# Performance work log

Hardware: AMD Instinct MI355X
Metric: run time of the kernel (lower is better)

Reference implementation:

```python
import jax, jax.numpy as jnp
import numpy as np

N, E, D_IN, HEADS, C = 100000, 1600000, 128, 4, 32  # C = out_channels per head


def setup_inputs() -> dict:
    key = jax.random.key(0)
    ks = jax.random.split(key, 10)
    s = 1.0 / np.sqrt(D_IN)
    return {
        "x": jax.random.normal(ks[0], (N, D_IN), jnp.float32),
        "edge_index": jax.random.randint(ks[1], (2, E), 0, N, jnp.int64),
        "Wq": jax.random.normal(ks[2], (D_IN, HEADS * C), jnp.float32) * s,
        "bq": jnp.zeros((HEADS * C,), jnp.float32),
        "Wk": jax.random.normal(ks[3], (D_IN, HEADS * C), jnp.float32) * s,
        "bk": jnp.zeros((HEADS * C,), jnp.float32),
        "Wv": jax.random.normal(ks[4], (D_IN, HEADS * C), jnp.float32) * s,
        "bv": jnp.zeros((HEADS * C,), jnp.float32),
        "Wskip": jax.random.normal(ks[5], (D_IN, HEADS * C), jnp.float32) * s,
        "bskip": jnp.zeros((HEADS * C,), jnp.float32),
    }


def reference(x, edge_index, Wq, bq, Wk, bk, Wv, bv, Wskip, bskip):
    n = x.shape[0]
    src, dst = edge_index[0], edge_index[1]  # message flows src (j) -> dst (i)
    q = (x @ Wq + bq).reshape(n, HEADS, C)
    k = (x @ Wk + bk).reshape(n, HEADS, C)
    v = (x @ Wv + bv).reshape(n, HEADS, C)

    # per-edge attention logits [E, H]
    alpha = jnp.einsum('ehc,ehc->eh', q[dst], k[src]) / jnp.sqrt(jnp.float32(C))

    # segment softmax over incoming edges of each target node
    m = jax.ops.segment_max(alpha, dst, num_segments=n)          # [N, H]
    p = jnp.exp(alpha - m[dst])                                   # [E, H]
    z = jax.ops.segment_sum(p, dst, num_segments=n)               # [N, H]
    w = p / (z[dst] + 1e-16)                                      # [E, H]

    # softmax-weighted scatter aggregation of values
    out = jax.ops.segment_sum(v[src] * w[:, :, None], dst, num_segments=n)
    out = out.reshape(n, HEADS * C)

    # root/skip connection (beta=False default: plain add)
    out = out + x @ Wskip + bskip
    return out
```

## Files before the change

kernel.cpp:

```cpp
#include <hip/hip_runtime.h>

#define DIN 128
#define NHEADS 4
#define CH 32
#define MT 64
#define NPB 256
#define EPB_IT 25
#define FB_CAP 6144

#define ST_H 136

typedef _Float16 h8 __attribute__((ext_vector_type(8)));
typedef _Float16 h2 __attribute__((ext_vector_type(2)));
typedef float f4 __attribute__((ext_vector_type(4)));

__global__ __launch_bounds__(256) void prep_w(
    const float* __restrict__ Wq, const float* __restrict__ Wk,
    const float* __restrict__ Wv, const float* __restrict__ Wsk,
    _Float16* __restrict__ wt)
{
    int i = blockIdx.x * 256 + threadIdx.x;
    if (i >= 4 * 16384) return;
    int mat = i >> 14;
    int rem = i & 16383;
    int n  = rem >> 7;
    int kk = rem & 127;
    const float* W = (mat == 0) ? Wq : (mat == 1) ? Wk : (mat == 2) ? Wv : Wsk;
    wt[i] = (_Float16)W[kk * 128 + n];
}

__global__ __launch_bounds__(256) void qkvs_mat(
    const float* __restrict__ x, const _Float16* __restrict__ wt,
    const float* __restrict__ bq, const float* __restrict__ bk,
    const float* __restrict__ bv, const float* __restrict__ bsk,
    _Float16* __restrict__ qh, _Float16* __restrict__ kh,
    _Float16* __restrict__ vh, _Float16* __restrict__ skiph, int N)
{
    __shared__ _Float16 Sbuf[MT * ST_H];
    const int t = threadIdx.x;
    const int mat = blockIdx.x;
    const int rowBase = blockIdx.y * MT;

    for (int i = t; i < MT * 16; i += 256) {
        int r  = i >> 4;
        int c8 = i & 15;
        int gr = rowBase + r;
        _Float16 h[8];
        if (gr < N) {
            float4 f0 = reinterpret_cast<const float4*>(x)[(size_t)gr * 32 + c8 * 2];
            float4 f1 = reinterpret_cast<const float4*>(x)[(size_t)gr * 32 + c8 * 2 + 1];
            h[0] = (_Float16)f0.x; h[1] = (_Float16)f0.y;
            h[2] = (_Float16)f0.z; h[3] = (_Float16)f0.w;
            h[4] = (_Float16)f1.x; h[5] = (_Float16)f1.y;
            h[6] = (_Float16)f1.z; h[7] = (_Float16)f1.w;
        } else {
            #pragma unroll
            for (int j = 0; j < 8; ++j) h[j] = (_Float16)0.f;
        }
        *reinterpret_cast<uint4*>(&Sbuf[r * 128 + ((c8 ^ (r & 7)) << 3)]) =
            *reinterpret_cast<uint4*>(h);
    }
    __syncthreads();

    const int wid  = t >> 6;
    const int l    = t & 63;
    const int lm   = l & 15;
    const int quad = l >> 4;

    const _Float16* __restrict__ Bsrc = wt + (size_t)mat * 16384;

    f4 acc[8];
    #pragma unroll
    for (int nt = 0; nt < 8; ++nt)
        acc[nt] = (f4){0.f, 0.f, 0.f, 0.f};

    #pragma unroll
    for (int kq = 0; kq < 4; ++kq) {
        const int c8 = kq * 4 + quad;
        const int k0 = c8 << 3;
        h8 a0 = *reinterpret_cast<const h8*>(
            &Sbuf[(wid * 16 + lm) * 128 + ((c8 ^ (lm & 7)) << 3)]);
        #pragma unroll
        for (int nt = 0; nt < 8; ++nt) {
            h8 b = *reinterpret_cast<const h8*>(
                &Bsrc[(size_t)(nt * 16 + lm) * 128 + k0]);
            acc[nt] = __builtin_amdgcn_mfma_f32_16x16x32_f16(a0, b, acc[nt], 0, 0, 0);
        }
    }
    __syncthreads();

    const float* bias = (mat == 0) ? bq : (mat == 1) ? bk : (mat == 2) ? bv : bsk;

    #pragma unroll
    for (int nt = 0; nt < 8; ++nt) {
        int col = nt * 16 + lm;
        float bsv = bias[col];
        int row = wid * 16 + quad * 4;
        #pragma unroll
        for (int i2 = 0; i2 < 4; ++i2)
            Sbuf[(row + i2) * ST_H + col] = (_Float16)(acc[nt][i2] + bsv);
    }
    __syncthreads();

    _Float16* __restrict__ dst = (mat == 0) ? qh : (mat == 1) ? kh
                               : (mat == 2) ? vh : skiph;
    for (int j = t; j < MT * 16; j += 256) {
        int r  = j >> 4;
        int c0 = (j & 15) << 3;
        int gr = rowBase + r;
        if (gr < N)
            *reinterpret_cast<uint4*>(&dst[(size_t)gr * 128 + c0]) =
                *reinterpret_cast<const uint4*>(&Sbuf[r * ST_H + c0]);
    }
}

__global__ __launch_bounds__(256) void bucket_hist(
    const int* __restrict__ ei, int* __restrict__ bcnt, int E, int nb)
{
    __shared__ int lds[512];
    for (int b = threadIdx.x; b < nb; b += 256) lds[b] = 0;
    __syncthreads();
    for (long long i = (long long)blockIdx.x * 256 + threadIdx.x; i < E;
         i += (long long)gridDim.x * 256)
        atomicAdd(&lds[ei[(size_t)E + i] >> 8], 1);
    __syncthreads();
    for (int b = threadIdx.x; b < nb; b += 256)
        if (lds[b]) atomicAdd(&bcnt[b], lds[b]);
}

__global__ __launch_bounds__(512) void scan_buckets(
    const int* __restrict__ bcnt, int* __restrict__ boff,
    int* __restrict__ bcur, int nb)
{
    __shared__ int ws[8];
    int t = threadIdx.x, lane = t & 63, wid = t >> 6;
    int v = (t < nb) ? bcnt[t] : 0;
    int s = v;
    #pragma unroll
    for (int off = 1; off < 64; off <<= 1) {
        int n = __shfl_up(s, off);
        if (lane >= off) s += n;
    }
    if (lane == 63) ws[wid] = s;
    __syncthreads();
    int add = 0;
    for (int w = 0; w < wid; ++w) add += ws[w];
    int excl = s - v + add;
    if (t < nb) { boff[t] = excl; bcur[t] = excl; }
    if (t == nb - 1) boff[nb] = excl + v;
}

__global__ __launch_bounds__(256) void bucket_scatter(
    const int* __restrict__ ei, int* __restrict__ bcur,
    unsigned* __restrict__ pairs, int E, int nb)
{
    __shared__ int cnt[512];
    int t = threadIdx.x;
    for (int b = t; b < nb; b += 256) cnt[b] = 0;
    __syncthreads();

    long long e0 = (long long)blockIdx.x * (256 * EPB_IT);
    int ps[EPB_IT], pd[EPB_IT];
    #pragma unroll
    for (int j = 0; j < EPB_IT; ++j) {
        long long e = e0 + j * 256 + t;
        if (e < E) {
            ps[j] = ei[e];
            pd[j] = ei[(size_t)E + e];
            atomicAdd(&cnt[pd[j] >> 8], 1);
        } else pd[j] = -1;
    }
    __syncthreads();
    for (int b = t; b < nb; b += 256) {
        int c = cnt[b];
        if (c) cnt[b] = atomicAdd(&bcur[b], c);
    }
    __syncthreads();
    #pragma unroll
    for (int j = 0; j < EPB_IT; ++j) {
        if (pd[j] >= 0) {
            int pos = atomicAdd(&cnt[pd[j] >> 8], 1);
            pairs[pos] = ((unsigned)ps[j] << 8) | ((unsigned)pd[j] & 255u);
        }
    }
}

__global__ __launch_bounds__(256) void bucket_finalize(
    const unsigned* __restrict__ pairs, const int* __restrict__ boff,
    int* __restrict__ rowptr, int* __restrict__ sorted, int N, int nb)
{
    __shared__ int cnt[NPB];
    __shared__ int cur[NPB];
    __shared__ int ws[4];
    __shared__ int sbuf[FB_CAP];
    int b = blockIdx.x, t = threadIdx.x;
    cnt[t] = 0;
    __syncthreads();
    int s0 = boff[b], e0 = boff[b + 1];
    int sz = e0 - s0;
    for (int i = s0 + t; i < e0; i += 256)
        atomicAdd(&cnt[pairs[i] & (NPB - 1)], 1);
    __syncthreads();

    int v = cnt[t];
    int lane = t & 63, wid = t >> 6;
    int incl = v;
    #pragma unroll
    for (int off = 1; off < 64; off <<= 1) {
        int n = __shfl_up(incl, off);
        if (lane >= off) incl += n;
    }
    if (lane == 63) ws[wid] = incl;
    __syncthreads();
    int add = 0;
    for (int w = 0; w < wid; ++w) add += ws[w];
    int lbase = (incl - v) + add;

    int node = b * NPB + t;
    if (node < N) rowptr[node] = s0 + lbase;
    if (b == nb - 1 && t == 0) rowptr[N] = boff[nb];
    cur[t] = lbase;
    __syncthreads();

    if (sz <= FB_CAP) {
        for (int i = s0 + t; i < e0; i += 256) {
            unsigned pr = pairs[i];
            int lpos = atomicAdd(&cur[pr & (NPB - 1)], 1);
            sbuf[lpos] = (int)(pr >> 8);
        }
        __syncthreads();
        for (int i = t; i < sz; i += 256)
            sorted[s0 + i] = sbuf[i];
    } else {
        for (int i = s0 + t; i < e0; i += 256) {
            unsigned pr = pairs[i];
            int pos = atomicAdd(&cur[pr & (NPB - 1)], 1);
            sorted[s0 + pos] = (int)(pr >> 8);
        }
    }
}

__device__ inline float4 cvt4(unsigned lo, unsigned hi) {
    union { unsigned u[2]; _Float16 h[4]; } c;
    c.u[0] = lo; c.u[1] = hi;
    return make_float4((float)c.h[0], (float)c.h[1], (float)c.h[2], (float)c.h[3]);
}

__device__ inline h2 as_h2(unsigned u) {
    union { unsigned u; h2 h; } c;
    c.u = u;
    return c.h;
}

__global__ __launch_bounds__(256) void node_aggregate(
    const _Float16* __restrict__ q, const _Float16* __restrict__ kh,
    const _Float16* __restrict__ vh, const _Float16* __restrict__ skiph,
    const int* __restrict__ rowptr, const int* __restrict__ srcs,
    float* __restrict__ out, int N)
{
    int gid  = blockIdx.x * 256 + threadIdx.x;
    int node = gid >> 5;
    if (node >= N) return;
    int l = gid & 31;

    uint2 qu = reinterpret_cast<const uint2*>(q + (size_t)node * 128)[l];
    h2 qa = as_h2(qu.x), qb = as_h2(qu.y);

    float4 acc = make_float4(0.f, 0.f, 0.f, 0.f);
    float z = 0.f;

    const uint2* k2 = reinterpret_cast<const uint2*>(kh);
    const uint2* v2 = reinterpret_cast<const uint2*>(vh);
    const float SC = 0.17677669529663687f;
    int e0 = rowptr[node], e1 = rowptr[node + 1];
    int e = e0;

    for (; e + 8 <= e1; e += 8) {
        int s[8];
        #pragma unroll
        for (int j = 0; j < 8; ++j) s[j] = srcs[e + j];
        uint2 kr[8], vr[8];
        #pragma unroll
        for (int j = 0; j < 8; ++j) kr[j] = k2[(size_t)s[j] * 32 + l];
        #pragma unroll
        for (int j = 0; j < 8; ++j) vr[j] = v2[(size_t)s[j] * 32 + l];

        float sv[8];
        #pragma unroll
        for (int j = 0; j < 8; ++j) {
            sv[j] = __builtin_amdgcn_fdot2(qa, as_h2(kr[j].x),
                    __builtin_amdgcn_fdot2(qb, as_h2(kr[j].y), 0.f, false), false);
        }
        #pragma unroll
        for (int j = 0; j < 8; ++j) sv[j] += __shfl_xor(sv[j], 1);
        #pragma unroll
        for (int j = 0; j < 8; ++j) sv[j] += __shfl_xor(sv[j], 2);
        #pragma unroll
        for (int j = 0; j < 8; ++j) sv[j] += __shfl_xor(sv[j], 4);

        #pragma unroll
        for (int j = 0; j < 8; ++j) {
            float p = __expf(sv[j] * SC);
            float4 v = cvt4(vr[j].x, vr[j].y);
            z += p;
            acc.x += p * v.x; acc.y += p * v.y;
            acc.z += p * v.z; acc.w += p * v.w;
        }
    }
    for (; e < e1; ++e) {
        int s0 = srcs[e];
        uint2 kr = k2[(size_t)s0 * 32 + l];
        uint2 vr = v2[(size_t)s0 * 32 + l];
        float sa = __builtin_amdgcn_fdot2(qa, as_h2(kr.x),
                   __builtin_amdgcn_fdot2(qb, as_h2(kr.y), 0.f, false), false);
        sa += __shfl_xor(sa, 1);
        sa += __shfl_xor(sa, 2);
        sa += __shfl_xor(sa, 4);
        float pa = __expf(sa * SC);
        float4 v0 = cvt4(vr.x, vr.y);
        z += pa;
        acc.x += pa * v0.x; acc.y += pa * v0.y;
        acc.z += pa * v0.z; acc.w += pa * v0.w;
    }

    uint2 su = reinterpret_cast<const uint2*>(skiph + (size_t)node * 128)[l];
    float4 sk = cvt4(su.x, su.y);
    float inv = 1.f / (z + 1e-16f);
    float4 o;
    o.x = sk.x + acc.x * inv; o.y = sk.y + acc.y * inv;
    o.z = sk.z + acc.z * inv; o.w = sk.w + acc.w * inv;
    reinterpret_cast<float4*>(out)[(size_t)node * 32 + l] = o;
}

extern "C" void kernel_launch(void* const* d_in, const int* in_sizes, int n_in,
                              void* d_out, int out_size, void* d_ws, size_t ws_size,
                              hipStream_t stream)
{
    const float* x   = (const float*)d_in[0];
    const int*   ei  = (const int*)d_in[1];
    const float* Wq  = (const float*)d_in[2];
    const float* bq  = (const float*)d_in[3];
    const float* Wk  = (const float*)d_in[4];
    const float* bk  = (const float*)d_in[5];
    const float* Wv  = (const float*)d_in[6];
    const float* bv  = (const float*)d_in[7];
    const float* Wsk = (const float*)d_in[8];
    const float* bsk = (const float*)d_in[9];
    float* out = (float*)d_out;

    const int N = in_sizes[0] / DIN;
    const int E = in_sizes[1] / 2;
    const int nb = (N + NPB - 1) / NPB;

    _Float16* qh    = (_Float16*)d_ws;
    _Float16* kh    = qh + (size_t)N * DIN;
    _Float16* vh    = kh + (size_t)N * DIN;
    _Float16* skiph = vh + (size_t)N * DIN;
    _Float16* wt    = skiph + (size_t)N * DIN;
    unsigned* pairs = (unsigned*)(wt + 4 * 16384);
    int* sorted   = (int*)(pairs + (size_t)E);
    int* rowptr   = sorted + E;
    int* bcnt     = rowptr + (N + 1);
    int* boff     = bcnt + 512;
    int* bcur     = boff + 513;

    hipMemsetAsync(bcnt, 0, 512 * sizeof(int), stream);

    prep_w<<<(4 * 16384 + 255) / 256, 256, 0, stream>>>(Wq, Wk, Wv, Wsk, wt);

    dim3 ggrid(4, (N + MT - 1) / MT);
    qkvs_mat<<<ggrid, 256, 0, stream>>>(x, wt, bq, bk, bv, bsk,
                                        qh, kh, vh, skiph, N);

    bucket_hist<<<256, 256, 0, stream>>>(ei, bcnt, E, nb);
    scan_buckets<<<1, 512, 0, stream>>>(bcnt, boff, bcur, nb);
    int sb = (E + 256 * EPB_IT - 1) / (256 * EPB_IT);
    bucket_scatter<<<sb, 256, 0, stream>>>(ei, bcur, pairs, E, nb);
    bucket_finalize<<<nb, 256, 0, stream>>>(pairs, boff, rowptr, sorted, N, nb);

    int ab = (N * 32 + 255) / 256;
    node_aggregate<<<ab, 256, 0, stream>>>(qh, kh, vh, skiph, rowptr, sorted, out, N);
}
```

Before: 404.4 us.

## Drop edge histogram pass by scattering into fixed-capacity destination buckets

Each 256-node bucket now gets a fixed 6144-slot region in the pairs buffer, so bucket_scatter no longer needs exact offsets from a prior histogram and scan. The bucket_hist kernel and its pass over the destination indices are removed. The scan now runs after the scatter, over the final per-bucket counts, to produce compact output offsets for bucket_finalize. This saves one kernel launch and one read of the edge destination array. In exchange it drops the large-bucket fallback: any bucket with more than 6144 incoming edges will overflow into the next region or LDS and give wrong results on skewed graphs.

```diff
diff --git a/kernel.cpp b/kernel.cpp
--- a/kernel.cpp
+++ b/kernel.cpp
@@ -6,7 +6,7 @@
 #define MT 64
 #define NPB 256
 #define EPB_IT 25
-#define FB_CAP 6144
+#define BCAP 6144
 
 #define ST_H 136
 
@@ -114,42 +114,6 @@
     }
 }
 
-__global__ __launch_bounds__(256) void bucket_hist(
-    const int* __restrict__ ei, int* __restrict__ bcnt, int E, int nb)
-{
-    __shared__ int lds[512];
-    for (int b = threadIdx.x; b < nb; b += 256) lds[b] = 0;
-    __syncthreads();
-    for (long long i = (long long)blockIdx.x * 256 + threadIdx.x; i < E;
-         i += (long long)gridDim.x * 256)
-        atomicAdd(&lds[ei[(size_t)E + i] >> 8], 1);
-    __syncthreads();
-    for (int b = threadIdx.x; b < nb; b += 256)
-        if (lds[b]) atomicAdd(&bcnt[b], lds[b]);
-}
-
-__global__ __launch_bounds__(512) void scan_buckets(
-    const int* __restrict__ bcnt, int* __restrict__ boff,
-    int* __restrict__ bcur, int nb)
-{
-    __shared__ int ws[8];
-    int t = threadIdx.x, lane = t & 63, wid = t >> 6;
-    int v = (t < nb) ? bcnt[t] : 0;
-    int s = v;
-    #pragma unroll
-    for (int off = 1; off < 64; off <<= 1) {
-        int n = __shfl_up(s, off);
-        if (lane >= off) s += n;
-    }
-    if (lane == 63) ws[wid] = s;
-    __syncthreads();
-    int add = 0;
-    for (int w = 0; w < wid; ++w) add += ws[w];
-    int excl = s - v + add;
-    if (t < nb) { boff[t] = excl; bcur[t] = excl; }
-    if (t == nb - 1) boff[nb] = excl + v;
-}
-
 __global__ __launch_bounds__(256) void bucket_scatter(
     const int* __restrict__ ei, int* __restrict__ bcur,
     unsigned* __restrict__ pairs, int E, int nb)
@@ -173,7 +137,7 @@
     __syncthreads();
     for (int b = t; b < nb; b += 256) {
         int c = cnt[b];
-        if (c) cnt[b] = atomicAdd(&bcur[b], c);
+        if (c) cnt[b] = b * BCAP + atomicAdd(&bcur[b], c);
     }
     __syncthreads();
     #pragma unroll
@@ -185,21 +149,44 @@
     }
 }
 
+__global__ __launch_bounds__(512) void scan_buckets(
+    const int* __restrict__ bcur, int* __restrict__ boff, int nb)
+{
+    __shared__ int ws[8];
+    int t = threadIdx.x, lane = t & 63, wid = t >> 6;
+    int v = (t < nb) ? bcur[t] : 0;
+    int s = v;
+    #pragma unroll
+    for (int off = 1; off < 64; off <<= 1) {
+        int n = __shfl_up(s, off);
+        if (lane >= off) s += n;
+    }
+    if (lane == 63) ws[wid] = s;
+    __syncthreads();
+    int add = 0;
+    for (int w = 0; w < wid; ++w) add += ws[w];
+    int excl = s - v + add;
+    if (t < nb) boff[t] = excl;
+    if (t == nb - 1) boff[nb] = excl + v;
+}
+
 __global__ __launch_bounds__(256) void bucket_finalize(
-    const unsigned* __restrict__ pairs, const int* __restrict__ boff,
+    const unsigned* __restrict__ pairs, const int* __restrict__ bcur,
+    const int* __restrict__ boff,
     int* __restrict__ rowptr, int* __restrict__ sorted, int N, int nb)
 {
     __shared__ int cnt[NPB];
     __shared__ int cur[NPB];
     __shared__ int ws[4];
-    __shared__ int sbuf[FB_CAP];
+    __shared__ int sbuf[BCAP];
     int b = blockIdx.x, t = threadIdx.x;
     cnt[t] = 0;
     __syncthreads();
-    int s0 = boff[b], e0 = boff[b + 1];
-    int sz = e0 - s0;
-    for (int i = s0 + t; i < e0; i += 256)
-        atomicAdd(&cnt[pairs[i] & (NPB - 1)], 1);
+    size_t r0 = (size_t)b * BCAP;
+    int sz = bcur[b];
+    int w0 = boff[b];
+    for (int i = t; i < sz; i += 256)
+        atomicAdd(&cnt[pairs[r0 + i] & (NPB - 1)], 1);
     __syncthreads();
 
     int v = cnt[t];
@@ -217,27 +204,19 @@
     int lbase = (incl - v) + add;
 
     int node = b * NPB + t;
-    if (node < N) rowptr[node] = s0 + lbase;
+    if (node < N) rowptr[node] = w0 + lbase;
     if (b == nb - 1 && t == 0) rowptr[N] = boff[nb];
     cur[t] = lbase;
     __syncthreads();
 
-    if (sz <= FB_CAP) {
-        for (int i = s0 + t; i < e0; i += 256) {
-            unsigned pr = pairs[i];
-            int lpos = atomicAdd(&cur[pr & (NPB - 1)], 1);
-            sbuf[lpos] = (int)(pr >> 8);
-        }
-        __syncthreads();
-        for (int i = t; i < sz; i += 256)
-            sorted[s0 + i] = sbuf[i];
-    } else {
-        for (int i = s0 + t; i < e0; i += 256) {
-            unsigned pr = pairs[i];
-            int pos = atomicAdd(&cur[pr & (NPB - 1)], 1);
-            sorted[s0 + pos] = (int)(pr >> 8);
-        }
-    }
+    for (int i = t; i < sz; i += 256) {
+        unsigned pr = pairs[r0 + i];
+        int lpos = atomicAdd(&cur[pr & (NPB - 1)], 1);
+        sbuf[lpos] = (int)(pr >> 8);
+    }
+    __syncthreads();
+    for (int i = t; i < sz; i += 256)
+        sorted[w0 + i] = sbuf[i];
 }
 
 __device__ inline float4 cvt4(unsigned lo, unsigned hi) {
@@ -358,13 +337,12 @@
     _Float16* skiph = vh + (size_t)N * DIN;
     _Float16* wt    = skiph + (size_t)N * DIN;
     unsigned* pairs = (unsigned*)(wt + 4 * 16384);
-    int* sorted   = (int*)(pairs + (size_t)E);
+    int* sorted   = (int*)(pairs + (size_t)nb * BCAP);
     int* rowptr   = sorted + E;
-    int* bcnt     = rowptr + (N + 1);
-    int* boff     = bcnt + 512;
-    int* bcur     = boff + 513;
-
-    hipMemsetAsync(bcnt, 0, 512 * sizeof(int), stream);
+    int* bcur     = rowptr + (N + 1);
+    int* boff     = bcur + 512;
+
+    hipMemsetAsync(bcur, 0, 512 * sizeof(int), stream);
 
     prep_w<<<(4 * 16384 + 255) / 256, 256, 0, stream>>>(Wq, Wk, Wv, Wsk, wt);
 
@@ -372,11 +350,10 @@
     qkvs_mat<<<ggrid, 256, 0, stream>>>(x, wt, bq, bk, bv, bsk,
                                         qh, kh, vh, skiph, N);
 
-    bucket_hist<<<256, 256, 0, stream>>>(ei, bcnt, E, nb);
-    scan_buckets<<<1, 512, 0, stream>>>(bcnt, boff, bcur, nb);
     int sb = (E + 256 * EPB_IT - 1) / (256 * EPB_IT);
     bucket_scatter<<<sb, 256, 0, stream>>>(ei, bcur, pairs, E, nb);
-    bucket_finalize<<<nb, 256, 0, stream>>>(pairs, boff, rowptr, sorted, N, nb);
+    scan_buckets<<<1, 512, 0, stream>>>(bcur, boff, nb);
+    bucket_finalize<<<nb, 256, 0, stream>>>(pairs, bcur, boff, rowptr, sorted, N, nb);
 
     int ab = (N * 32 + 255) / 256;
     node_aggregate<<<ab, 256, 0, stream>>>(qh, kh, vh, skiph, rowptr, sorted, out, N);
```

Measured after the change: 389.0 us. -3.8%, faster.
